# Performance work log

Hardware: AMD Instinct MI355X
Metric: run time of the kernel (lower is better)

## Reference

```python
import jax, jax.numpy as jnp
import numpy as np

N_NODES = 256
BATCH = 1024
N_LAYERS = 2  # total linear layers = N_LAYERS + 1, each followed by tanh


def setup_inputs() -> dict:
    key = jax.random.key(0)
    ks = jax.random.split(key, 4)
    scale = 1.0 / np.sqrt(N_NODES)
    x = jax.random.normal(ks[0], (BATCH, N_NODES), dtype=jnp.float32)
    # nn.Linear weights: [out_features, in_features], no bias
    W0 = jax.random.normal(ks[1], (N_NODES, N_NODES), dtype=jnp.float32) * scale
    W1 = jax.random.normal(ks[2], (N_NODES, N_NODES), dtype=jnp.float32) * scale
    W2 = jax.random.normal(ks[3], (N_NODES, N_NODES), dtype=jnp.float32) * scale
    return {"x": x, "W0": W0, "W1": W1, "W2": W2}


def reference(x, W0, W1, W2):
    # Original loop: for each node i, zero out column i of x (x @ Par with
    # Par = I - e_i e_i^T), run the 3-layer tanh MLP, keep output column i.
    # Vectorized: build all N masked copies at once.
    N = x.shape[1]
    mask = (1.0 - jnp.eye(N, dtype=x.dtype))  # [i, j]: zero col j==i
    Xm = x[None, :, :] * mask[:, None, :]     # [N, B, N]
    # nn.Linear: y = h @ W.T ; tanh after every layer (incl. last)
    h = jnp.tanh(jnp.einsum('ibn,mn->ibm', Xm, W0))
    h = jnp.tanh(jnp.einsum('ibn,mn->ibm', h, W1))
    h = jnp.tanh(jnp.einsum('ibn,mn->ibm', h, W2))  # [N, B, N]
    # f_x[b, i] = h[i, b, i]
    f_x = jnp.einsum('ibi->bi', h)
    return f_x
```

## Files before the change

kernel.cpp:

```cpp
#include <hip/hip_runtime.h>
#include <hip/hip_bf16.h>

#define N_NODES 256
#define BATCH   1024

typedef __attribute__((ext_vector_type(8))) short bf16x8;
typedef __attribute__((ext_vector_type(4))) float f32x4;

__device__ __forceinline__ float ftanh(float x) {
    float e = __builtin_amdgcn_exp2f(x * 2.8853900817779268f);
    float r = __builtin_amdgcn_rcpf(e + 1.0f);
    return fmaf(-2.0f, r, 1.0f);
}

__device__ __forceinline__ unsigned short f2bf(float f) {
    unsigned u = __float_as_uint(f);
    return (unsigned short)((u + 0x7fffu + ((u >> 16) & 1u)) >> 16);
}

__device__ __forceinline__ unsigned pack_bf2(float a, float b) {
    union { __hip_bfloat162 h; unsigned u; } cvt;
    cvt.h = __float22bfloat162_rn(make_float2(a, b));
    return cvt.u;
}

__global__ void z0_prep(const float* __restrict__ x, const float* __restrict__ W0,
                        const float* __restrict__ W1, float* __restrict__ Z0,
                        float* __restrict__ xT, float* __restrict__ W0col,
                        unsigned short* __restrict__ W1bf) {
    __shared__ float xs[32][36];
    __shared__ float ws[32][36];
    int t = threadIdx.x;

    int gb = (blockIdx.y * 32 + blockIdx.x) * 256 + t;
    {
        int i = gb >> 8, m = gb & 255;
        W0col[gb] = W0[m * 256 + i];
        W1bf[gb]  = f2bf(W1[gb]);
    }
#pragma unroll
    for (int r = 0; r < 4; ++r) {
        int id = r * 65536 + gb;
        int i = id >> 10, b = id & 1023;
        xT[id] = x[b * 256 + i];
    }

    int b0 = blockIdx.x * 32, m0 = blockIdx.y * 32;
    int lr = t >> 3, lc = (t & 7) << 2;
    int tr = (t >> 4) << 1, tc = (t & 15) << 1;
    float acc00 = 0.f, acc01 = 0.f, acc10 = 0.f, acc11 = 0.f;
    for (int k0 = 0; k0 < 256; k0 += 32) {
        *(float4*)&xs[lr][lc] = *(const float4*)&x[(b0 + lr) * 256 + k0 + lc];
        *(float4*)&ws[lr][lc] = *(const float4*)&W0[(m0 + lr) * 256 + k0 + lc];
        __syncthreads();
#pragma unroll
        for (int k = 0; k < 32; ++k) {
            float a0 = xs[tr][k], a1 = xs[tr + 1][k];
            float w0v = ws[tc][k], w1v = ws[tc + 1][k];
            acc00 = fmaf(a0, w0v, acc00);
            acc01 = fmaf(a0, w1v, acc01);
            acc10 = fmaf(a1, w0v, acc10);
            acc11 = fmaf(a1, w1v, acc11);
        }
        __syncthreads();
    }
    Z0[(b0 + tr) * 256 + m0 + tc]         = acc00;
    Z0[(b0 + tr) * 256 + m0 + tc + 1]     = acc01;
    Z0[(b0 + tr + 1) * 256 + m0 + tc]     = acc10;
    Z0[(b0 + tr + 1) * 256 + m0 + tc + 1] = acc11;
}

__launch_bounds__(256, 4)
__global__ void fused(const float* __restrict__ Z0, const float* __restrict__ xT,
                      const float* __restrict__ W0col,
                      const unsigned short* __restrict__ W1bf,
                      const float* __restrict__ W2, float* __restrict__ out) {
    __shared__ __align__(16) unsigned char h0s[64 * 512];
    float* wavepart = (float*)h0s;
    int t  = threadIdx.x;
    int r0 = blockIdx.x * 64;
    int i  = blockIdx.y;

    int wave = t >> 6, lane = t & 63;
    int lr = lane & 15, lh = lane >> 4;

    float w2v[4];
#pragma unroll
    for (int nt = 0; nt < 4; ++nt)
        w2v[nt] = W2[i * 256 + wave * 64 + nt * 16 + lr];

    {
        int rowgrp = t >> 5, chunk = t & 31;
        int col0 = chunk << 3;
        float4 w0a = *(const float4*)&W0col[i * 256 + col0];
        float4 w0b = *(const float4*)&W0col[i * 256 + col0 + 4];
        float w[8] = {w0a.x, w0a.y, w0a.z, w0a.w, w0b.x, w0b.y, w0b.z, w0b.w};
#pragma unroll
        for (int p = 0; p < 8; ++p) {
            int row = p * 8 + rowgrp;
            float xi = xT[i * 1024 + r0 + row];
            float4 za = *(const float4*)&Z0[(r0 + row) * 256 + col0];
            float4 zb = *(const float4*)&Z0[(r0 + row) * 256 + col0 + 4];
            float z[8] = {za.x, za.y, za.z, za.w, zb.x, zb.y, zb.z, zb.w};
            unsigned pk[4];
#pragma unroll
            for (int e = 0; e < 4; ++e) {
                float ha = ftanh(fmaf(-xi, w[2 * e],     z[2 * e]));
                float hb = ftanh(fmaf(-xi, w[2 * e + 1], z[2 * e + 1]));
                pk[e] = pack_bf2(ha, hb);
            }
            uint4 v = make_uint4(pk[0], pk[1], pk[2], pk[3]);
            *(uint4*)(h0s + row * 512 + (((chunk ^ (row & 31)) << 4))) = v;
        }
    }
    __syncthreads();

    f32x4 acc[4][4];
#pragma unroll
    for (int a = 0; a < 4; ++a)
#pragma unroll
        for (int b = 0; b < 4; ++b)
            acc[a][b] = (f32x4){0.f, 0.f, 0.f, 0.f};

#pragma unroll
    for (int ks = 0; ks < 8; ++ks) {
        int kk = ks * 32 + lh * 8;
        int chunk = kk >> 3;
        bf16x8 afrag[4], bfrag[4];
#pragma unroll
        for (int mt = 0; mt < 4; ++mt) {
            int row = mt * 16 + lr;
            afrag[mt] = *(const bf16x8*)(h0s + row * 512 + ((chunk ^ (row & 31)) << 4));
        }
#pragma unroll
        for (int nt = 0; nt < 4; ++nt) {
            int j = wave * 64 + nt * 16 + lr;
            bfrag[nt] = *(const bf16x8*)(W1bf + j * 256 + kk);
        }
#pragma unroll
        for (int mt = 0; mt < 4; ++mt)
#pragma unroll
            for (int nt = 0; nt < 4; ++nt)
                acc[mt][nt] = __builtin_amdgcn_mfma_f32_16x16x32_bf16(
                    afrag[mt], bfrag[nt], acc[mt][nt], 0, 0, 0);
    }

    float part[4][4];
#pragma unroll
    for (int mt = 0; mt < 4; ++mt) {
#pragma unroll
        for (int r = 0; r < 4; ++r) {
            float s = 0.f;
#pragma unroll
            for (int nt = 0; nt < 4; ++nt)
                s = fmaf(ftanh(acc[mt][nt][r]), w2v[nt], s);
            s += __shfl_xor(s, 1);
            s += __shfl_xor(s, 2);
            s += __shfl_xor(s, 4);
            s += __shfl_xor(s, 8);
            part[mt][r] = s;
        }
    }
    __syncthreads();
    if (lr == 0) {
#pragma unroll
        for (int mt = 0; mt < 4; ++mt)
#pragma unroll
            for (int r = 0; r < 4; ++r)
                wavepart[wave * 64 + mt * 16 + lh * 4 + r] = part[mt][r];
    }
    __syncthreads();

    if (t < 64) {
        float s = wavepart[t] + wavepart[64 + t] + wavepart[128 + t] + wavepart[192 + t];
        out[(r0 + t) * 256 + i] = ftanh(s);
    }
}

extern "C" void kernel_launch(void* const* d_in, const int* in_sizes, int n_in,
                              void* d_out, int out_size, void* d_ws, size_t ws_size,
                              hipStream_t stream) {
    const float* x  = (const float*)d_in[0];
    const float* W0 = (const float*)d_in[1];
    const float* W1 = (const float*)d_in[2];
    const float* W2 = (const float*)d_in[3];
    float* out = (float*)d_out;

    char* ws = (char*)d_ws;
    float* Z0            = (float*)ws;
    float* xT            = (float*)(ws + (1 << 20));
    float* W0col         = (float*)(ws + (2 << 20));
    unsigned short* W1bf = (unsigned short*)(ws + (2 << 20) + (256 << 10));

    z0_prep<<<dim3(32, 8), 256, 0, stream>>>(x, W0, W1, Z0, xT, W0col, W1bf);
    fused<<<dim3(16, 256), 256, 0, stream>>>(Z0, xT, W0col, W1bf, W2, out);
}
```

Baseline: 89.57 us.

## Pad LDS rows, prefetch W1 fragments, and use DPP row reductions

Replaces the XOR-swizzled LDS layout for h0 with padded 528-byte rows, which simplifies address math while still avoiding bank conflicts. W1 B-fragments are software-prefetched one k-step ahead in registers to hide global load latency behind the MFMAs. The cross-lane reduction switches from shfl_xor to DPP row_shr adds, with lane 15 writing the partial into a separate wavepart buffer, which also removes one __syncthreads. The cost is more LDS (about 34 KB plus 1 KB) and extra registers from the prefetch, both of which may reduce occupancy.

```diff
diff --git a/kernel.cpp b/kernel.cpp
--- a/kernel.cpp
+++ b/kernel.cpp
@@ -3,6 +3,7 @@
 
 #define N_NODES 256
 #define BATCH   1024
+#define ROWB    528
 
 typedef __attribute__((ext_vector_type(8))) short bf16x8;
 typedef __attribute__((ext_vector_type(4))) float f32x4;
@@ -22,6 +23,12 @@
     union { __hip_bfloat162 h; unsigned u; } cvt;
     cvt.h = __float22bfloat162_rn(make_float2(a, b));
     return cvt.u;
+}
+
+template <int CTRL>
+__device__ __forceinline__ float dpp_add(float s) {
+    int t = __builtin_amdgcn_update_dpp(0, __float_as_int(s), CTRL, 0xf, 0xf, true);
+    return s + __int_as_float(t);
 }
 
 __global__ void z0_prep(const float* __restrict__ x, const float* __restrict__ W0,
@@ -75,14 +82,14 @@
                       const float* __restrict__ W0col,
                       const unsigned short* __restrict__ W1bf,
                       const float* __restrict__ W2, float* __restrict__ out) {
-    __shared__ __align__(16) unsigned char h0s[64 * 512];
-    float* wavepart = (float*)h0s;
-    int t  = threadIdx.x;
-    int r0 = blockIdx.x * 64;
-    int i  = blockIdx.y;
-
-    int wave = t >> 6, lane = t & 63;
-    int lr = lane & 15, lh = lane >> 4;
+    __shared__ __align__(16) unsigned char h0s[64 * ROWB];
+    __shared__ float wavepart[4 * 64];
+    const int t  = threadIdx.x;
+    const int r0 = blockIdx.x * 64;
+    const int i  = blockIdx.y;
+
+    const int wave = t >> 6, lane = t & 63;
+    const int lr = lane & 15, lh = lane >> 4;
 
     float w2v[4];
 #pragma unroll
@@ -90,8 +97,9 @@
         w2v[nt] = W2[i * 256 + wave * 64 + nt * 16 + lr];
 
     {
-        int rowgrp = t >> 5, chunk = t & 31;
-        int col0 = chunk << 3;
+        const int rowgrp = t >> 5, chunk = t & 31;
+        const int col0 = chunk << 3;
+        unsigned char* wbase = h0s + rowgrp * ROWB + chunk * 16;
         float4 w0a = *(const float4*)&W0col[i * 256 + col0];
         float4 w0b = *(const float4*)&W0col[i * 256 + col0 + 4];
         float w[8] = {w0a.x, w0a.y, w0a.z, w0a.w, w0b.x, w0b.y, w0b.z, w0b.w};
@@ -109,8 +117,7 @@
                 float hb = ftanh(fmaf(-xi, w[2 * e + 1], z[2 * e + 1]));
                 pk[e] = pack_bf2(ha, hb);
             }
-            uint4 v = make_uint4(pk[0], pk[1], pk[2], pk[3]);
-            *(uint4*)(h0s + row * 512 + (((chunk ^ (row & 31)) << 4))) = v;
+            *(uint4*)(wbase + p * 8 * ROWB) = make_uint4(pk[0], pk[1], pk[2], pk[3]);
         }
     }
     __syncthreads();
@@ -122,21 +129,33 @@
         for (int b = 0; b < 4; ++b)
             acc[a][b] = (f32x4){0.f, 0.f, 0.f, 0.f};
 
+    const unsigned char* abase[4];
+#pragma unroll
+    for (int mt = 0; mt < 4; ++mt)
+        abase[mt] = h0s + (mt * 16 + lr) * ROWB + lh * 16;
+
+    const unsigned short* w1p[4];
+#pragma unroll
+    for (int nt = 0; nt < 4; ++nt)
+        w1p[nt] = W1bf + (wave * 64 + nt * 16 + lr) * 256 + lh * 8;
+    bf16x8 bnext[4];
+#pragma unroll
+    for (int nt = 0; nt < 4; ++nt)
+        bnext[nt] = *(const bf16x8*)(w1p[nt]);
+
 #pragma unroll
     for (int ks = 0; ks < 8; ++ks) {
-        int kk = ks * 32 + lh * 8;
-        int chunk = kk >> 3;
-        bf16x8 afrag[4], bfrag[4];
-#pragma unroll
-        for (int mt = 0; mt < 4; ++mt) {
-            int row = mt * 16 + lr;
-            afrag[mt] = *(const bf16x8*)(h0s + row * 512 + ((chunk ^ (row & 31)) << 4));
-        }
+        bf16x8 bfrag[4];
 #pragma unroll
         for (int nt = 0; nt < 4; ++nt) {
-            int j = wave * 64 + nt * 16 + lr;
-            bfrag[nt] = *(const bf16x8*)(W1bf + j * 256 + kk);
-        }
+            bfrag[nt] = bnext[nt];
+            if (ks < 7)
+                bnext[nt] = *(const bf16x8*)(w1p[nt] + (ks + 1) * 32);
+        }
+        bf16x8 afrag[4];
+#pragma unroll
+        for (int mt = 0; mt < 4; ++mt)
+            afrag[mt] = *(const bf16x8*)(abase[mt] + ks * 64);
 #pragma unroll
         for (int mt = 0; mt < 4; ++mt)
 #pragma unroll
@@ -145,29 +164,21 @@
                     afrag[mt], bfrag[nt], acc[mt][nt], 0, 0, 0);
     }
 
-    float part[4][4];
 #pragma unroll
     for (int mt = 0; mt < 4; ++mt) {
 #pragma unroll
         for (int r = 0; r < 4; ++r) {
-            float s = 0.f;
-#pragma unroll
-            for (int nt = 0; nt < 4; ++nt)
-                s = fmaf(ftanh(acc[mt][nt][r]), w2v[nt], s);
-            s += __shfl_xor(s, 1);
-            s += __shfl_xor(s, 2);
-            s += __shfl_xor(s, 4);
-            s += __shfl_xor(s, 8);
-            part[mt][r] = s;
-        }
-    }
-    __syncthreads();
-    if (lr == 0) {
-#pragma unroll
-        for (int mt = 0; mt < 4; ++mt)
-#pragma unroll
-            for (int r = 0; r < 4; ++r)
-                wavepart[wave * 64 + mt * 16 + lh * 4 + r] = part[mt][r];
+            float s = fmaf(ftanh(acc[mt][0][r]), w2v[0],
+                           ftanh(acc[mt][1][r]) * w2v[1]);
+            s = fmaf(ftanh(acc[mt][2][r]), w2v[2], s);
+            s = fmaf(ftanh(acc[mt][3][r]), w2v[3], s);
+            s = dpp_add<0x118>(s);
+            s = dpp_add<0x114>(s);
+            s = dpp_add<0x112>(s);
+            s = dpp_add<0x111>(s);
+            if (lr == 15)
+                wavepart[wave * 64 + mt * 16 + lh * 4 + r] = s;
+        }
     }
     __syncthreads();
 
```

After: 87.80 us (median of 4 runs). 1.02x faster.
